# Kernel optimization log

Hardware: AMD Instinct MI355X
Metric: run time of the kernel (lower is better)

## Reference

```python
import jax, jax.numpy as jnp
import numpy as np

D_MODEL = 1024
N_HEADS = 16
HEAD_DIM = D_MODEL // N_HEADS
WINDOW = 256
NEG_INF = -1e30  # finite stand-in for -inf; identical softmax result, NaN-safe


def setup_inputs() -> dict:
    key = jax.random.key(0)
    ks = jax.random.split(key, 5)
    B, L = 1, 4096
    s = 1.0 / np.sqrt(D_MODEL)
    return {
        "x": jax.random.normal(ks[0], (B, L, D_MODEL), dtype=jnp.float32),
        "Wq": jax.random.normal(ks[1], (D_MODEL, D_MODEL), dtype=jnp.float32) * s,
        "Wk": jax.random.normal(ks[2], (D_MODEL, D_MODEL), dtype=jnp.float32) * s,
        "Wv": jax.random.normal(ks[3], (D_MODEL, D_MODEL), dtype=jnp.float32) * s,
        "Wo": jax.random.normal(ks[4], (D_MODEL, D_MODEL), dtype=jnp.float32) * s,
    }


def reference(x, Wq, Wk, Wv, Wo):
    B, L, _ = x.shape
    # projections (nn.Linear applies x @ W.T; weights here are stored as [out,in])
    q = (x @ Wq.T).reshape(B, L, N_HEADS, HEAD_DIM).transpose(0, 2, 1, 3)  # [B,H,L,Dh]
    k = (x @ Wk.T).reshape(B, L, N_HEADS, HEAD_DIM).transpose(0, 2, 1, 3)
    v = (x @ Wv.T).reshape(B, L, N_HEADS, HEAD_DIM).transpose(0, 2, 1, 3)

    # sliding-window causal mask: position i attends to j in [i-WINDOW+1, i]
    i = jnp.arange(L)[:, None]
    j = jnp.arange(L)[None, :]
    allowed = (j <= i) & (j >= i - WINDOW + 1)  # [L,L] bool

    scale = 1.0 / jnp.sqrt(jnp.asarray(HEAD_DIM, dtype=q.dtype))
    scores = jnp.einsum("bhqd,bhkd->bhqk", q, k) * scale  # [B,H,L,L]
    scores = jnp.where(allowed, scores, NEG_INF)
    attn = jax.nn.softmax(scores, axis=-1)
    out = jnp.einsum("bhqk,bhkd->bhqd", attn, v)  # [B,H,L,Dh]
    out = out.transpose(0, 2, 1, 3).reshape(B, L, D_MODEL)
    return out @ Wo.T
```

## Files before the change

kernel.cpp:

```cpp
#include <hip/hip_runtime.h>

using bf16x8 = __attribute__((ext_vector_type(8))) short;
using u16x8  = __attribute__((ext_vector_type(8))) unsigned short;
using f32x4  = __attribute__((ext_vector_type(4))) float;

#define LSEQ   4096
#define NH     16
#define DH     64
#define WIN    256
#define DM     1024

__device__ __forceinline__ void gl2lds16(const void* g, void* l) {
  __builtin_amdgcn_global_load_lds(
      (const __attribute__((address_space(1))) unsigned int*)g,
      (__attribute__((address_space(3))) unsigned int*)l,
      16, 0, 0);
}

__device__ __forceinline__ unsigned short f2bf(float f) {
  unsigned int u = __float_as_uint(f);
  u += 0x7fffu + ((u >> 16) & 1u);
  return (unsigned short)(u >> 16);
}

__global__ __launch_bounds__(256) void cvt_all(
    const float* __restrict__ x,  const float* __restrict__ wq,
    const float* __restrict__ wk, const float* __restrict__ wv,
    const float* __restrict__ wo, unsigned short* __restrict__ dst)
{
  const size_t i = ((size_t)blockIdx.x * 256 + threadIdx.x) * 8;
  const size_t XN = (size_t)LSEQ * DM;
  const float* src;
  size_t off;
  if (i < XN) { src = x; off = i; }
  else {
    const size_t j = i - XN;
    const int s = (int)(j >> 20);
    off = j & ((1u << 20) - 1);
    src = (s == 0) ? wq : (s == 1) ? wk : (s == 2) ? wv : wo;
  }
  const f32x4 f0 = *(const f32x4*)(src + off);
  const f32x4 f1 = *(const f32x4*)(src + off + 4);
  u16x8 o;
  o[0] = f2bf(f0[0]); o[1] = f2bf(f0[1]); o[2] = f2bf(f0[2]); o[3] = f2bf(f0[3]);
  o[4] = f2bf(f1[0]); o[5] = f2bf(f1[1]); o[6] = f2bf(f1[2]); o[7] = f2bf(f1[3]);
  *(u16x8*)(dst + i) = o;
}

__device__ __forceinline__ void gemm_tile_db8(
    const unsigned short* __restrict__ X,
    const unsigned short* __restrict__ W,
    int m0, int n0,
    unsigned short* As0, unsigned short* Bs0,
    f32x4 (&acc)[4][2])
{
  const int tid  = threadIdx.x;
  const int lane = tid & 63;
  const int wave = tid >> 6;
  const int wm = wave >> 2;
  const int wn = wave & 3;
  const int fr = lane & 15, quad = lane >> 4;
  const int sw = fr & 7;

  const f32x4 zero = {0.f, 0.f, 0.f, 0.f};
  #pragma unroll
  for (int i = 0; i < 4; ++i)
    #pragma unroll
    for (int j = 0; j < 2; ++j)
      acc[i][j] = zero;

  const unsigned short* ga[2];
  const unsigned short* gb[2];
  int lc[2];
  #pragma unroll
  for (int cc = 0; cc < 2; ++cc) {
    const int c = tid + cc * 512;
    const int row = c >> 3;
    const int gp  = (c & 7) ^ (row & 7);
    ga[cc] = X + (size_t)(m0 + row) * DM + gp * 8;
    gb[cc] = W + (size_t)(n0 + row) * DM + gp * 8;
    lc[cc] = c * 16;
  }
  char* laA = (char*)As0;
  char* laB = (char*)Bs0;

  #pragma unroll
  for (int cc = 0; cc < 2; ++cc) {
    gl2lds16(ga[cc], laA + lc[cc]);
    gl2lds16(gb[cc], laB + lc[cc]);
  }
  __syncthreads();

  #define PITER(KT, CUR, NXT)                                                 \
    do {                                                                      \
      if ((KT) + 64 < DM) {                                                   \
        _Pragma("unroll")                                                     \
        for (int cc = 0; cc < 2; ++cc) {                                      \
          gl2lds16(ga[cc] + (KT) + 64, laA + (NXT) * 16384 + lc[cc]);         \
          gl2lds16(gb[cc] + (KT) + 64, laB + (NXT) * 16384 + lc[cc]);         \
        }                                                                     \
      }                                                                       \
      const unsigned short* As_ = As0 + (CUR) * 8192;                         \
      const unsigned short* Bs_ = Bs0 + (CUR) * 8192;                         \
      _Pragma("unroll")                                                       \
      for (int s = 0; s < 2; ++s) {                                           \
        bf16x8 a[4], b[2];                                                    \
        _Pragma("unroll")                                                     \
        for (int t = 0; t < 4; ++t)                                           \
          a[t] = *(const bf16x8*)(As_ + (wm * 64 + t * 16 + fr) * 64          \
                                      + (((s * 4 + quad) ^ sw) * 8));         \
        _Pragma("unroll")                                                     \
        for (int t = 0; t < 2; ++t)                                           \
          b[t] = *(const bf16x8*)(Bs_ + (wn * 32 + t * 16 + fr) * 64          \
                                      + (((s * 4 + quad) ^ sw) * 8));         \
        __builtin_amdgcn_s_setprio(1);                                        \
        _Pragma("unroll")                                                     \
        for (int i = 0; i < 4; ++i)                                           \
          _Pragma("unroll")                                                   \
          for (int j = 0; j < 2; ++j)                                         \
            acc[i][j] = __builtin_amdgcn_mfma_f32_16x16x32_bf16(              \
                a[i], b[j], acc[i][j], 0, 0, 0);                              \
        __builtin_amdgcn_s_setprio(0);                                        \
      }                                                                       \
      __syncthreads();                                                        \
    } while (0)

  #pragma unroll 1
  for (int kt2 = 0; kt2 < DM; kt2 += 128) {
    PITER(kt2,      0, 1);
    PITER(kt2 + 64, 1, 0);
  }
  #undef PITER
}

__global__ __launch_bounds__(512) void proj_gemm(
    const unsigned short* __restrict__ X,
    const unsigned short* __restrict__ Wq,
    const unsigned short* __restrict__ Wk,
    const unsigned short* __restrict__ Wv,
    unsigned short* __restrict__ Qo,
    unsigned short* __restrict__ Ko,
    unsigned short* __restrict__ Vt)
{
  __shared__ __align__(16) unsigned short As[2 * 128 * 64];
  __shared__ __align__(16) unsigned short Bs[2 * 128 * 64];
  const int id = blockIdx.x;
  const int lane = threadIdx.x & 63;
  const int wave = threadIdx.x >> 6;
  const int wm = wave >> 2, wn = wave & 3;
  const int cn = lane & 15, quad = lane >> 4;
  f32x4 acc[4][2];

  if (id < 512) {
    const int m0   = (id & 31) * 128;
    const int by   = id >> 5;
    const int wsel = by >> 3;
    const int n0   = (by & 7) * 128;
    gemm_tile_db8(X, wsel ? Wk : Wq, m0, n0, As, Bs, acc);

    const float qscl = wsel ? 1.0f : 0.180336881f;
    unsigned short* O = wsel ? Ko : Qo;
    #pragma unroll
    for (int i = 0; i < 4; ++i)
      #pragma unroll
      for (int j = 0; j < 2; ++j)
        #pragma unroll
        for (int r = 0; r < 4; ++r) {
          const int row = m0 + wm * 64 + i * 16 + quad * 4 + r;
          const int col = n0 + wn * 32 + j * 16 + cn;
          const int h = col >> 6, d = col & 63;
          O[(size_t)(h * LSEQ + row) * DH + d] = f2bf(acc[i][j][r] * qscl);
        }
  } else {
    const int vid = id - 512;
    const int m0 = (vid & 7) * 128;
    const int n0 = (vid >> 3) * 128;
    gemm_tile_db8(Wv, X, m0, n0, As, Bs, acc);

    #pragma unroll
    for (int i = 0; i < 4; ++i)
      #pragma unroll
      for (int j = 0; j < 2; ++j)
        #pragma unroll
        for (int r = 0; r < 4; ++r) {
          const int row = m0 + wm * 64 + i * 16 + quad * 4 + r;
          const int col = n0 + wn * 32 + j * 16 + cn;
          Vt[(size_t)row * LSEQ + col] = f2bf(acc[i][j][r]);
        }
  }
}

__global__ __launch_bounds__(256) void out_gemm(
    const unsigned short* __restrict__ X,
    const unsigned short* __restrict__ W,
    float* __restrict__ O)
{
  __shared__ __align__(16) unsigned short As2[2 * 64 * 64];
  __shared__ __align__(16) unsigned short Bs[2 * 128 * 64];
  const int m0 = blockIdx.x * 64;
  const int n0 = blockIdx.y * 128;
  const int tid  = threadIdx.x;
  const int lane = tid & 63;
  const int wave = tid >> 6;
  const int wm = wave >> 1, wn = wave & 1;
  const int fr = lane & 15, quad = lane >> 4;
  const int sw = fr & 7;

  const f32x4 zero = {0.f, 0.f, 0.f, 0.f};
  f32x4 acc[2][4];
  #pragma unroll
  for (int i = 0; i < 2; ++i)
    #pragma unroll
    for (int j = 0; j < 4; ++j)
      acc[i][j] = zero;

  const unsigned short* ga[2];
  int lca[2];
  #pragma unroll
  for (int cc = 0; cc < 2; ++cc) {
    const int c = tid + cc * 256;
    const int row = c >> 3;
    const int gpp = (c & 7) ^ (row & 7);
    ga[cc] = X + (size_t)(m0 + row) * DM + gpp * 8;
    lca[cc] = c * 16;
  }
  const unsigned short* gb[4];
  int lcb[4];
  #pragma unroll
  for (int cc = 0; cc < 4; ++cc) {
    const int c = tid + cc * 256;
    const int row = c >> 3;
    const int gpp = (c & 7) ^ (row & 7);
    gb[cc] = W + (size_t)(n0 + row) * DM + gpp * 8;
    lcb[cc] = c * 16;
  }
  char* laA = (char*)As2;
  char* laB = (char*)Bs;

  #pragma unroll
  for (int cc = 0; cc < 2; ++cc) gl2lds16(ga[cc], laA + lca[cc]);
  #pragma unroll
  for (int cc = 0; cc < 4; ++cc) gl2lds16(gb[cc], laB + lcb[cc]);
  __syncthreads();

  #define OITER(KT, CUR, NXT)                                                 \
    do {                                                                      \
      if ((KT) + 64 < DM) {                                                   \
        _Pragma("unroll")                                                     \
        for (int cc = 0; cc < 2; ++cc)                                        \
          gl2lds16(ga[cc] + (KT) + 64, laA + (NXT) * 8192 + lca[cc]);         \
        _Pragma("unroll")                                                     \
        for (int cc = 0; cc < 4; ++cc)                                        \
          gl2lds16(gb[cc] + (KT) + 64, laB + (NXT) * 16384 + lcb[cc]);        \
      }                                                                       \
      const unsigned short* As_ = As2 + (CUR) * 4096;                         \
      const unsigned short* Bs_ = Bs + (CUR) * 8192;                          \
      _Pragma("unroll")                                                       \
      for (int s = 0; s < 2; ++s) {                                           \
        bf16x8 a[2], b[4];                                                    \
        _Pragma("unroll")                                                     \
        for (int t = 0; t < 2; ++t)                                           \
          a[t] = *(const bf16x8*)(As_ + (wm * 32 + t * 16 + fr) * 64          \
                                      + (((s * 4 + quad) ^ sw) * 8));         \
        _Pragma("unroll")                                                     \
        for (int t = 0; t < 4; ++t)                                           \
          b[t] = *(const bf16x8*)(Bs_ + (wn * 64 + t * 16 + fr) * 64          \
                                      + (((s * 4 + quad) ^ sw) * 8));         \
        __builtin_amdgcn_s_setprio(1);                                        \
        _Pragma("unroll")                                                     \
        for (int i = 0; i < 2; ++i)                                           \
          _Pragma("unroll")                                                   \
          for (int j = 0; j < 4; ++j)                                         \
            acc[i][j] = __builtin_amdgcn_mfma_f32_16x16x32_bf16(              \
                a[i], b[j], acc[i][j], 0, 0, 0);                              \
        __builtin_amdgcn_s_setprio(0);                                        \
      }                                                                       \
      __syncthreads();                                                        \
    } while (0)

  #pragma unroll 1
  for (int kt2 = 0; kt2 < DM; kt2 += 128) {
    OITER(kt2,      0, 1);
    OITER(kt2 + 64, 1, 0);
  }
  #undef OITER

  const int cn = lane & 15;
  #pragma unroll
  for (int i = 0; i < 2; ++i)
    #pragma unroll
    for (int j = 0; j < 4; ++j)
      #pragma unroll
      for (int r = 0; r < 4; ++r) {
        const int row = m0 + wm * 32 + i * 16 + quad * 4 + r;
        const int col = n0 + wn * 64 + j * 16 + cn;
        O[(size_t)row * DM + col] = acc[i][j][r];
      }
}

#define PSTR 72
__global__ __launch_bounds__(512) void attn_fwd(
    const unsigned short* __restrict__ Q,
    const unsigned short* __restrict__ K,
    const unsigned short* __restrict__ Vt,
    unsigned short* __restrict__ Oa)
{
  __shared__ unsigned short Ks[2][64 * PSTR];
  __shared__ unsigned short Vs[2][64 * PSTR];
  __shared__ unsigned short Pl[8][16 * PSTR];
  const int id   = blockIdx.x;
  const int h    = (id & 7) | ((id >> 8) << 3);
  const int bq0  = ((id >> 3) & 31) * 128;
  const int tid  = threadIdx.x;
  const int wave = tid >> 6;
  const int lane = tid & 63;
  const int n = lane & 15, quad = lane >> 4;
  const int q0 = bq0 + wave * 16;
  unsigned short* pl = Pl[wave];

  const size_t qbase = ((size_t)(h * LSEQ + q0 + n)) * DH + quad * 8;
  const bf16x8 aq0 = *(const bf16x8*)(Q + qbase);
  const bf16x8 aq1 = *(const bf16x8*)(Q + qbase + 32);

  const int lo = (bq0 >= WIN) ? (bq0 - WIN) : 0;
  const int hi = bq0 + 128;

  const int krow = tid >> 3, part = tid & 7;
  const size_t kg = ((size_t)(h * LSEQ + krow)) * DH + part * 8;
  const size_t vg = ((size_t)(h * DH + krow)) * LSEQ + part * 8;
  const int ld = krow * PSTR + part * 8;

  {
    *(bf16x8*)(Ks[0] + ld) = *(const bf16x8*)(K  + kg + (size_t)lo * DH);
    *(bf16x8*)(Vs[0] + ld) = *(const bf16x8*)(Vt + vg + lo);
  }
  __syncthreads();

  const f32x4 zero = {0.f, 0.f, 0.f, 0.f};
  f32x4 acc[4] = {zero, zero, zero, zero};
  float li[4] = {0.f, 0.f, 0.f, 0.f};

  int t = 0;
  for (int jb = lo; jb < hi; jb += 64, ++t) {
    const int buf = t & 1;
    const bool more = (jb + 64 < hi);
    bf16x8 nk, nv;
    if (more) {
      nk = *(const bf16x8*)(K  + kg + (size_t)(jb + 64) * DH);
      nv = *(const bf16x8*)(Vt + vg + (jb + 64));
    }
    const bool active = (jb <= q0 + 15) && (jb + 63 >= q0 - (WIN - 1));
    if (active) {
      const unsigned short* ks = Ks[buf];
      const unsigned short* vs = Vs[buf];
      f32x4 s[4];
      __builtin_amdgcn_s_setprio(1);
      #pragma unroll
      for (int u = 0; u < 4; ++u) {
        const bf16x8 kb0 = *(const bf16x8*)(ks + (u * 16 + n) * PSTR + quad * 8);
        const bf16x8 kb1 = *(const bf16x8*)(ks + (u * 16 + n) * PSTR + 32 + quad * 8);
        f32x4 c = zero;
        c = __builtin_amdgcn_mfma_f32_16x16x32_bf16(aq0, kb0, c, 0, 0, 0);
        c = __builtin_amdgcn_mfma_f32_16x16x32_bf16(aq1, kb1, c, 0, 0, 0);
        s[u] = c;
      }
      __builtin_amdgcn_s_setprio(0);
      const bool nomask = (jb + 63 <= q0) && (jb >= q0 + 15 - (WIN - 1));
      if (nomask) {
        #pragma unroll
        for (int u = 0; u < 4; ++u)
          #pragma unroll
          for (int r = 0; r < 4; ++r) {
            const float e = __builtin_exp2f(s[u][r] - 32.0f);
            s[u][r] = e;
            li[r] += e;
          }
      } else {
        #pragma unroll
        for (int u = 0; u < 4; ++u)
          #pragma unroll
          for (int r = 0; r < 4; ++r) {
            const int qi = q0 + quad * 4 + r;
            const int kj = jb + u * 16 + n;
            const bool ok = (kj <= qi) && (kj + WIN > qi);
            const float e = __builtin_exp2f(ok ? s[u][r] - 32.0f : -1e30f);
            s[u][r] = e;
            li[r] += e;
          }
      }
      #pragma unroll
      for (int u = 0; u < 4; ++u)
        #pragma unroll
        for (int r = 0; r < 4; ++r)
          pl[(quad * 4 + r) * PSTR + u * 16 + n] = f2bf(s[u][r]);
      asm volatile("s_waitcnt lgkmcnt(0)" ::: "memory");
      const bf16x8 pa0 = *(const bf16x8*)(pl + n * PSTR + quad * 8);
      const bf16x8 pa1 = *(const bf16x8*)(pl + n * PSTR + 32 + quad * 8);
      __builtin_amdgcn_s_setprio(1);
      #pragma unroll
      for (int ct = 0; ct < 4; ++ct) {
        const bf16x8 vb0 = *(const bf16x8*)(vs + (ct * 16 + n) * PSTR + quad * 8);
        const bf16x8 vb1 = *(const bf16x8*)(vs + (ct * 16 + n) * PSTR + 32 + quad * 8);
        acc[ct] = __builtin_amdgcn_mfma_f32_16x16x32_bf16(pa0, vb0, acc[ct], 0, 0, 0);
        acc[ct] = __builtin_amdgcn_mfma_f32_16x16x32_bf16(pa1, vb1, acc[ct], 0, 0, 0);
      }
      __builtin_amdgcn_s_setprio(0);
    }
    if (more) {
      *(bf16x8*)(Ks[buf ^ 1] + ld) = nk;
      *(bf16x8*)(Vs[buf ^ 1] + ld) = nv;
    }
    __syncthreads();
  }

  float rd[4];
  #pragma unroll
  for (int r = 0; r < 4; ++r) {
    float v = li[r];
    v += __shfl_xor(v, 1);
    v += __shfl_xor(v, 2);
    v += __shfl_xor(v, 4);
    v += __shfl_xor(v, 8);
    rd[r] = 1.0f / v;
  }
  #pragma unroll
  for (int ct = 0; ct < 4; ++ct)
    #pragma unroll
    for (int r = 0; r < 4; ++r) {
      const int row = q0 + quad * 4 + r;
      const int col = h * DH + ct * 16 + n;
      Oa[(size_t)row * DM + col] = f2bf(acc[ct][r] * rd[r]);
    }
}

extern "C" void kernel_launch(void* const* d_in, const int* in_sizes, int n_in,
                              void* d_out, int out_size, void* d_ws, size_t ws_size,
                              hipStream_t stream) {
  const float* x  = (const float*)d_in[0];
  const float* Wq = (const float*)d_in[1];
  const float* Wk = (const float*)d_in[2];
  const float* Wv = (const float*)d_in[3];
  const float* Wo = (const float*)d_in[4];
  float* out = (float*)d_out;

  unsigned short* xb  = (unsigned short*)d_ws;
  unsigned short* Wqb = xb  + (size_t)LSEQ * DM;
  unsigned short* Wkb = Wqb + (size_t)DM * DM;
  unsigned short* Wvb = Wkb + (size_t)DM * DM;
  unsigned short* Wob = Wvb + (size_t)DM * DM;
  unsigned short* Q    = Wob + (size_t)DM * DM;
  unsigned short* K    = Q   + (size_t)LSEQ * DM;
  unsigned short* Vt   = K   + (size_t)LSEQ * DM;
  unsigned short* Attn = Vt  + (size_t)LSEQ * DM;

  cvt_all<<<dim3(4096), 256, 0, stream>>>(x, Wq, Wk, Wv, Wo, xb);
  proj_gemm<<<dim3(768), 512, 0, stream>>>(xb, Wqb, Wkb, Wvb, Q, K, Vt);
  attn_fwd<<<dim3(512), 512, 0, stream>>>(Q, K, Vt, Attn);
  out_gemm<<<dim3(64, 8), 256, 0, stream>>>(Attn, Wob, out);
}
```

Before: 152.4 us.

## Fuse fp32-to-bf16 conversion of x into projection GEMM tile loads

The separate pass that converts x to bf16 is removed. The projection GEMM now loads fp32 x tiles into registers, converts them, and writes them to LDS after the MFMA block, while weights still use direct global-to-LDS loads. This saves writing and re-reading a bf16 copy of x. In exchange, each of the many tiles that share an x row re-reads fp32 x at twice the bytes and redoes the conversion, and register pressure rises.

```diff
diff --git a/kernel.cpp b/kernel.cpp
--- a/kernel.cpp
+++ b/kernel.cpp
@@ -23,22 +23,15 @@
   return (unsigned short)(u >> 16);
 }
 
-__global__ __launch_bounds__(256) void cvt_all(
-    const float* __restrict__ x,  const float* __restrict__ wq,
-    const float* __restrict__ wk, const float* __restrict__ wv,
-    const float* __restrict__ wo, unsigned short* __restrict__ dst)
+__global__ __launch_bounds__(256) void cvt_w(
+    const float* __restrict__ wq, const float* __restrict__ wk,
+    const float* __restrict__ wv, const float* __restrict__ wo,
+    unsigned short* __restrict__ dst)
 {
   const size_t i = ((size_t)blockIdx.x * 256 + threadIdx.x) * 8;
-  const size_t XN = (size_t)LSEQ * DM;
-  const float* src;
-  size_t off;
-  if (i < XN) { src = x; off = i; }
-  else {
-    const size_t j = i - XN;
-    const int s = (int)(j >> 20);
-    off = j & ((1u << 20) - 1);
-    src = (s == 0) ? wq : (s == 1) ? wk : (s == 2) ? wv : wo;
-  }
+  const int s = (int)(i >> 20);
+  const size_t off = i & ((1u << 20) - 1);
+  const float* src = (s == 0) ? wq : (s == 1) ? wk : (s == 2) ? wv : wo;
   const f32x4 f0 = *(const f32x4*)(src + off);
   const f32x4 f1 = *(const f32x4*)(src + off + 4);
   u16x8 o;
@@ -47,9 +40,10 @@
   *(u16x8*)(dst + i) = o;
 }
 
-__device__ __forceinline__ void gemm_tile_db8(
-    const unsigned short* __restrict__ X,
-    const unsigned short* __restrict__ W,
+template<bool XA>
+__device__ __forceinline__ void gemm_tile_f32(
+    const float* __restrict__ Xg,
+    const unsigned short* __restrict__ Wg,
     int m0, int n0,
     unsigned short* As0, unsigned short* Bs0,
     f32x4 (&acc)[4][2])
@@ -69,35 +63,54 @@
     for (int j = 0; j < 2; ++j)
       acc[i][j] = zero;
 
-  const unsigned short* ga[2];
-  const unsigned short* gb[2];
+  const int x0 = XA ? m0 : n0;
+  const int w0 = XA ? n0 : m0;
+  unsigned short* Fb = XA ? As0 : Bs0;
+  char* Wb = (char*)(XA ? Bs0 : As0);
+
+  const float* gx[2];
+  const unsigned short* gw[2];
   int lc[2];
+  int ls[2];
   #pragma unroll
   for (int cc = 0; cc < 2; ++cc) {
     const int c = tid + cc * 512;
     const int row = c >> 3;
     const int gp  = (c & 7) ^ (row & 7);
-    ga[cc] = X + (size_t)(m0 + row) * DM + gp * 8;
-    gb[cc] = W + (size_t)(n0 + row) * DM + gp * 8;
+    gx[cc] = Xg + (size_t)(x0 + row) * DM + gp * 8;
+    gw[cc] = Wg + (size_t)(w0 + row) * DM + gp * 8;
     lc[cc] = c * 16;
-  }
-  char* laA = (char*)As0;
-  char* laB = (char*)Bs0;
-
-  #pragma unroll
-  for (int cc = 0; cc < 2; ++cc) {
-    gl2lds16(ga[cc], laA + lc[cc]);
-    gl2lds16(gb[cc], laB + lc[cc]);
+    ls[cc] = c * 8;
+  }
+
+  {
+    f32x4 xr[2][2];
+    #pragma unroll
+    for (int cc = 0; cc < 2; ++cc) {
+      xr[cc][0] = *(const f32x4*)(gx[cc]);
+      xr[cc][1] = *(const f32x4*)(gx[cc] + 4);
+      gl2lds16(gw[cc], Wb + lc[cc]);
+    }
+    #pragma unroll
+    for (int cc = 0; cc < 2; ++cc) {
+      u16x8 o;
+      #pragma unroll
+      for (int e = 0; e < 4; ++e) { o[e] = f2bf(xr[cc][0][e]); o[e+4] = f2bf(xr[cc][1][e]); }
+      *(u16x8*)(Fb + ls[cc]) = o;
+    }
   }
   __syncthreads();
 
   #define PITER(KT, CUR, NXT)                                                 \
     do {                                                                      \
-      if ((KT) + 64 < DM) {                                                   \
+      f32x4 xr[2][2];                                                         \
+      const bool more_ = (KT) + 64 < DM;                                      \
+      if (more_) {                                                            \
         _Pragma("unroll")                                                     \
         for (int cc = 0; cc < 2; ++cc) {                                      \
-          gl2lds16(ga[cc] + (KT) + 64, laA + (NXT) * 16384 + lc[cc]);         \
-          gl2lds16(gb[cc] + (KT) + 64, laB + (NXT) * 16384 + lc[cc]);         \
+          xr[cc][0] = *(const f32x4*)(gx[cc] + (KT) + 64);                    \
+          xr[cc][1] = *(const f32x4*)(gx[cc] + (KT) + 64 + 4);                \
+          gl2lds16(gw[cc] + (KT) + 64, Wb + (NXT) * 16384 + lc[cc]);          \
         }                                                                     \
       }                                                                       \
       const unsigned short* As_ = As0 + (CUR) * 8192;                         \
@@ -122,6 +135,16 @@
                 a[i], b[j], acc[i][j], 0, 0, 0);                              \
         __builtin_amdgcn_s_setprio(0);                                        \
       }                                                                       \
+      if (more_) {                                                            \
+        _Pragma("unroll")                                                     \
+        for (int cc = 0; cc < 2; ++cc) {                                      \
+          u16x8 o;                                                            \
+          _Pragma("unroll")                                                   \
+          for (int e = 0; e < 4; ++e) { o[e] = f2bf(xr[cc][0][e]);            \
+                                        o[e+4] = f2bf(xr[cc][1][e]); }        \
+          *(u16x8*)(Fb + (NXT) * 8192 + ls[cc]) = o;                          \
+        }                                                                     \
+      }                                                                       \
       __syncthreads();                                                        \
     } while (0)
 
@@ -134,7 +157,7 @@
 }
 
 __global__ __launch_bounds__(512) void proj_gemm(
-    const unsigned short* __restrict__ X,
+    const float* __restrict__ X,
     const unsigned short* __restrict__ Wq,
     const unsigned short* __restrict__ Wk,
     const unsigned short* __restrict__ Wv,
@@ -156,7 +179,7 @@
     const int by   = id >> 5;
     const int wsel = by >> 3;
     const int n0   = (by & 7) * 128;
-    gemm_tile_db8(X, wsel ? Wk : Wq, m0, n0, As, Bs, acc);
+    gemm_tile_f32<true>(X, wsel ? Wk : Wq, m0, n0, As, Bs, acc);
 
     const float qscl = wsel ? 1.0f : 0.180336881f;
     unsigned short* O = wsel ? Ko : Qo;
@@ -175,7 +198,7 @@
     const int vid = id - 512;
     const int m0 = (vid & 7) * 128;
     const int n0 = (vid >> 3) * 128;
-    gemm_tile_db8(Wv, X, m0, n0, As, Bs, acc);
+    gemm_tile_f32<false>(X, Wv, m0, n0, As, Bs, acc);
 
     #pragma unroll
     for (int i = 0; i < 4; ++i)
@@ -443,8 +466,7 @@
   const float* Wo = (const float*)d_in[4];
   float* out = (float*)d_out;
 
-  unsigned short* xb  = (unsigned short*)d_ws;
-  unsigned short* Wqb = xb  + (size_t)LSEQ * DM;
+  unsigned short* Wqb = (unsigned short*)d_ws;
   unsigned short* Wkb = Wqb + (size_t)DM * DM;
   unsigned short* Wvb = Wkb + (size_t)DM * DM;
   unsigned short* Wob = Wvb + (size_t)DM * DM;
@@ -453,8 +475,8 @@
   unsigned short* Vt   = K   + (size_t)LSEQ * DM;
   unsigned short* Attn = Vt  + (size_t)LSEQ * DM;
 
-  cvt_all<<<dim3(4096), 256, 0, stream>>>(x, Wq, Wk, Wv, Wo, xb);
-  proj_gemm<<<dim3(768), 512, 0, stream>>>(xb, Wqb, Wkb, Wvb, Q, K, Vt);
+  cvt_w<<<dim3(2048), 256, 0, stream>>>(Wq, Wk, Wv, Wo, Wqb);
+  proj_gemm<<<dim3(768), 512, 0, stream>>>(x, Wqb, Wkb, Wvb, Q, K, Vt);
   attn_fwd<<<dim3(512), 512, 0, stream>>>(Q, K, Vt, Attn);
   out_gemm<<<dim3(64, 8), 256, 0, stream>>>(Attn, Wob, out);
 }
```

Measured after the change: 178.2 us. 1.17x slower.
